# Kernel optimization log

Hardware: AMD Instinct MI355X
Metric: run time of the kernel (lower is better)

## Reference

```python
import jax, jax.numpy as jnp
import numpy as np

B, T, LAGS, H, F = 4096, 256, 32, 128, 2


def setup_inputs() -> dict:
    key = jax.random.key(0)
    ks = jax.random.split(key, 6)
    s = lambda n: 1.0 / np.sqrt(n)
    return {
        "inputs": jax.random.normal(ks[0], (B, T, F), jnp.float32),
        "Wx": jax.random.normal(ks[1], (F, H), jnp.float32) * s(F),
        "Wh": jax.random.normal(ks[2], (H, H), jnp.float32) * s(H),
        "b": jnp.zeros((H,), jnp.float32),
        "Wd": jax.random.normal(ks[3], (H, 1), jnp.float32) * s(H),
        "bd": jnp.zeros((1,), jnp.float32),
        "alpha": jax.random.uniform(ks[4], (1, 1), jnp.float32),
        "lags": LAGS,
    }


def reference(inputs, Wx, Wh, b, Wd, bd, alpha, lags):
    # alpha constrained to [0, 1] (MinMax constraint / clamp in call)
    a = jnp.clip(alpha, 0.0, 1.0)  # [1,1]
    Bsz = inputs.shape[0]
    h0 = jnp.zeros((Bsz, Wh.shape[0]), inputs.dtype)

    def cell(h, x):
        # SimpleRNN cell: tanh(x Wx + h Wh + b)
        return jnp.tanh(x @ Wx + h @ Wh + b)

    # ---- warmup: run RNN over first `lags` steps of the full 2-feature input
    warm_xs = jnp.transpose(inputs[:, :lags], (1, 0, 2))  # [lags, B, F]

    def warm_step(h, x):
        return cell(h, x), None

    h, _ = jax.lax.scan(warm_step, h0, warm_xs)
    pred = h @ Wd + bd  # [B, 1] first prediction (appended un-smoothed)

    # step n consumes exogenous inputs[:, lags + n - 1, 0]
    exog = jnp.transpose(inputs[:, lags:-1, 0])  # [T-lags-1, B]

    def ar_step(carry, e):
        h, pred, es = carry
        x = jnp.concatenate([e[:, None], pred], axis=-1)  # [B, 2]
        h = cell(h, x)
        pred = h @ Wd + bd
        es = a * pred + (1.0 - a) * es  # exponential smoothing blend
        return (h, pred, es), es

    _, es_seq = jax.lax.scan(ar_step, (h, pred, pred), exog)  # [T-lags-1, B, 1]

    preds = jnp.concatenate([pred[None], es_seq], axis=0)  # [T-lags, B, 1]
    return jnp.transpose(preds, (1, 0, 2))  # [B, T-lags, 1]
```

## Files before the change

### kernel.cpp

```cpp
#include <hip/hip_runtime.h>

namespace {

constexpr int kB = 4096;
constexpr int kT = 256;
constexpr int kLags = 32;
constexpr int kH = 128;
constexpr int kSteps = 255;
constexpr int kOut = 224;
constexpr int kMT = 16;
constexpr int kThreads = 512;
constexpr int kHS = 136;
constexpr int kOS = 225;

constexpr float kZS = 2.8853900817779268f;

typedef __attribute__((ext_vector_type(8))) short short8;
typedef __attribute__((ext_vector_type(4))) float f32x4;

struct __align__(16) SMem {
    unsigned short hhi[2][kMT][kHS];
    unsigned short hlo[2][kMT][kHS];
    float x0T[kT][kMT];
    float x1wT[kLags][kMT];
    float obuf[kMT][kOS];
};

__device__ __forceinline__ unsigned short bf16_rne(float f) {
    unsigned u = __builtin_bit_cast(unsigned, f);
    u += 0x7FFFu + ((u >> 16) & 1u);
    return (unsigned short)(u >> 16);
}
__device__ __forceinline__ float bf16_f32(unsigned short h) {
    unsigned u = ((unsigned)h) << 16;
    return __builtin_bit_cast(float, u);
}
__device__ __forceinline__ float tanh_from_zs(float zs) {
    float e = __builtin_amdgcn_exp2f(zs);
    return fmaf(-2.0f, __builtin_amdgcn_rcpf(e + 1.0f), 1.0f);
}
__device__ __forceinline__ unsigned bf16_rne_hibits(float f) {
    unsigned u = __builtin_bit_cast(unsigned, f);
    return (u + (0x7FFFu + ((u >> 16) & 1u))) & 0xFFFF0000u;
}

__global__ __launch_bounds__(kThreads, 2)
void arx_rnn_es_kernel(const float* __restrict__ inputs,
                       const float* __restrict__ Wx,
                       const float* __restrict__ Wh,
                       const float* __restrict__ bias,
                       const float* __restrict__ Wd,
                       const float* __restrict__ bd,
                       const float* __restrict__ alpha,
                       float* __restrict__ out) {
    __shared__ SMem sm;
    const int tid  = threadIdx.x;
    const int b0   = blockIdx.x * kMT;
    const int lane = tid & 63;
    const int w    = tid >> 6;
    const int n    = lane & 15;
    const int q    = lane >> 4;

    for (int idx = tid; idx < kMT * kT; idx += kThreads) {
        const int mm = idx >> 8;
        const int t  = idx & 255;
        float2 v = ((const float2*)inputs)[(size_t)(b0 + mm) * kT + t];
        sm.x0T[t][mm] = v.x;
        if (t < kLags) sm.x1wT[t][mm] = v.y;
    }
    for (int idx = tid; idx < kMT * kHS; idx += kThreads) {
        ((unsigned short*)sm.hhi[0])[idx] = 0;
        ((unsigned short*)sm.hlo[0])[idx] = 0;
    }

    const float av  = fminf(fmaxf(alpha[0], 0.0f), 1.0f);
    const float bdv = bd[0];

    float sb2[4], swx0[4], swx1e[4], sbp[4];
#pragma unroll
    for (int r = 0; r < 4; ++r) {
        const int colE = w * 16 + q * 4 + r;
        const float bc = bias[colE];
        const float w0 = Wx[colE];
        const float w1 = Wx[kH + colE];
        sb2[r]   = kZS * bc;
        swx0[r]  = kZS * w0;
        swx1e[r] = kZS * w1;
        sbp[r]   = kZS * (bc + bdv * w1);
    }
    __syncthreads();

    int p = 0;

    {
        short8 whh[4], whl[4];
        {
            const int colw = w * 16 + n;
#pragma unroll
            for (int c = 0; c < 4; ++c) {
#pragma unroll
                for (int j = 0; j < 8; ++j) {
                    const int k = c * 32 + q * 8 + j;
                    float wv = kZS * Wh[(size_t)k * kH + colw];
                    unsigned short hi = bf16_rne(wv);
                    whh[c][j] = (short)hi;
                    whl[c][j] = (short)bf16_rne(wv - bf16_f32(hi));
                }
            }
        }

#pragma unroll 1
        for (int st = 0; st < kLags; ++st) {
            const float x0s = sm.x0T[st][n];
            const float x1s = sm.x1wT[st][n];

            short8 bh[4], bl[4];
#pragma unroll
            for (int c = 0; c < 4; ++c) {
                bh[c] = *(const short8*)&sm.hhi[p][n][c * 32 + 8 * q];
                bl[c] = *(const short8*)&sm.hlo[p][n][c * 32 + 8 * q];
            }

            f32x4 A = *(const f32x4*)&sb2[0];
#pragma unroll
            for (int c = 0; c < 4; ++c) {
                A = __builtin_amdgcn_mfma_f32_16x16x32_bf16(whh[c], bh[c], A, 0, 0, 0);
                A = __builtin_amdgcn_mfma_f32_16x16x32_bf16(whl[c], bh[c], A, 0, 0, 0);
                A = __builtin_amdgcn_mfma_f32_16x16x32_bf16(whh[c], bl[c], A, 0, 0, 0);
            }

            unsigned rb[4], db[4];
#pragma unroll
            for (int r = 0; r < 4; ++r) {
                float zs = A[r] + x0s * swx0[r] + x1s * swx1e[r];
                float hf = tanh_from_zs(zs);
                rb[r] = bf16_rne_hibits(hf);
                float d = hf - __builtin_bit_cast(float, rb[r]);
                db[r] = __builtin_bit_cast(unsigned, d);
            }
            uint2 uh, ul;
            uh.x = __builtin_amdgcn_perm(rb[1], rb[0], 0x07060302u);
            uh.y = __builtin_amdgcn_perm(rb[3], rb[2], 0x07060302u);
            ul.x = __builtin_amdgcn_perm(db[1], db[0], 0x07060302u);
            ul.y = __builtin_amdgcn_perm(db[3], db[2], 0x07060302u);
            const int wcol = w * 16 + q * 4;
            *(uint2*)&sm.hhi[1 - p][n][wcol] = uh;
            *(uint2*)&sm.hlo[1 - p][n][wcol] = ul;

            __syncthreads();
            p ^= 1;
        }
    }

    short8 fhh[4], fhl[4], dh[4];
    {
        const int colw = w * 16 + n;
        const float wx1w = Wx[kH + colw];
#pragma unroll
        for (int c = 0; c < 4; ++c) {
#pragma unroll
            for (int j = 0; j < 8; ++j) {
                const int k = c * 32 + q * 8 + j;
                float wv = kZS * fmaf(Wd[k], wx1w, Wh[(size_t)k * kH + colw]);
                unsigned short hi = bf16_rne(wv);
                fhh[c][j] = (short)hi;
                fhl[c][j] = (short)bf16_rne(wv - bf16_f32(hi));
                dh[c][j]  = (short)bf16_rne(Wd[k]);
            }
        }
    }

    float es = 0.0f;

#pragma unroll 1
    for (int st = kLags; st < kSteps; ++st) {
        const float x0s = sm.x0T[st][n];

        short8 bh[4], bl[4];
#pragma unroll
        for (int c = 0; c < 4; ++c) {
            bh[c] = *(const short8*)&sm.hhi[p][n][c * 32 + 8 * q];
            bl[c] = *(const short8*)&sm.hlo[p][n][c * 32 + 8 * q];
        }

        f32x4 A = *(const f32x4*)&sbp[0];
        f32x4 P = {0, 0, 0, 0};
#pragma unroll
        for (int c = 0; c < 4; ++c) {
            A = __builtin_amdgcn_mfma_f32_16x16x32_bf16(fhh[c], bh[c], A, 0, 0, 0);
            A = __builtin_amdgcn_mfma_f32_16x16x32_bf16(fhl[c], bh[c], A, 0, 0, 0);
            A = __builtin_amdgcn_mfma_f32_16x16x32_bf16(fhh[c], bl[c], A, 0, 0, 0);
            if (w == 0)
                P = __builtin_amdgcn_mfma_f32_16x16x32_bf16(dh[c], bh[c], P, 0, 0, 0);
        }

        if (w == 0 && q == 0) {
            float pv = P[0] + bdv;
            es = (st == kLags) ? pv : fmaf(av, pv - es, es);
            sm.obuf[n][st - kLags] = es;
        }

        unsigned rb[4], db[4];
#pragma unroll
        for (int r = 0; r < 4; ++r) {
            float zs = A[r] + x0s * swx0[r];
            float hf = tanh_from_zs(zs);
            rb[r] = bf16_rne_hibits(hf);
            float d = hf - __builtin_bit_cast(float, rb[r]);
            db[r] = __builtin_bit_cast(unsigned, d);
        }
        uint2 uh, ul;
        uh.x = __builtin_amdgcn_perm(rb[1], rb[0], 0x07060302u);
        uh.y = __builtin_amdgcn_perm(rb[3], rb[2], 0x07060302u);
        ul.x = __builtin_amdgcn_perm(db[1], db[0], 0x07060302u);
        ul.y = __builtin_amdgcn_perm(db[3], db[2], 0x07060302u);
        const int wcol = w * 16 + q * 4;
        *(uint2*)&sm.hhi[1 - p][n][wcol] = uh;
        *(uint2*)&sm.hlo[1 - p][n][wcol] = ul;

        __syncthreads();
        p ^= 1;
    }

    if (w == 0) {
        f32x4 P = {0, 0, 0, 0};
#pragma unroll
        for (int c = 0; c < 4; ++c) {
            short8 bh = *(const short8*)&sm.hhi[p][n][c * 32 + 8 * q];
            P = __builtin_amdgcn_mfma_f32_16x16x32_bf16(dh[c], bh, P, 0, 0, 0);
        }
        if (q == 0) {
            float pv = P[0] + bdv;
            es = fmaf(av, pv - es, es);
            sm.obuf[n][kOut - 1] = es;
        }
    }

    __syncthreads();
    for (int idx = tid; idx < kMT * kOut; idx += kThreads) {
        const int mm = idx / kOut;
        const int t  = idx - mm * kOut;
        out[(size_t)(b0 + mm) * kOut + t] = sm.obuf[mm][t];
    }
}

}

extern "C" void kernel_launch(void* const* d_in, const int* in_sizes, int n_in,
                              void* d_out, int out_size, void* d_ws, size_t ws_size,
                              hipStream_t stream) {
    const float* inputs = (const float*)d_in[0];
    const float* Wx     = (const float*)d_in[1];
    const float* Wh     = (const float*)d_in[2];
    const float* bias   = (const float*)d_in[3];
    const float* Wd     = (const float*)d_in[4];
    const float* bd     = (const float*)d_in[5];
    const float* alpha  = (const float*)d_in[6];

    arx_rnn_es_kernel<<<kB / kMT, kThreads, 0, stream>>>(
        inputs, Wx, Wh, bias, Wd, bd, alpha, (float*)d_out);
}
```

Measured before the change: 206.0 us.

## Halve block to 4 waves, each computing two 16-column hidden tiles

The block shrinks from 8 to 4 wavefronts. Each wave now owns 32 hidden columns as two MFMA tiles, and both tiles reuse the same loaded h fragments from LDS. This halves the per-step LDS reads of h and the number of waves meeting at each per-step barrier, and gives two independent MFMA accumulation chains per wave to hide latency. In exchange, register pressure roughly doubles for the weight fragments, the launch_bounds occupancy hint is dropped, and fewer waves are available to hide latency on the serial recurrence.

```diff
diff --git a/kernel.cpp b/kernel.cpp
--- a/kernel.cpp
+++ b/kernel.cpp
@@ -9,7 +9,7 @@
 constexpr int kSteps = 255;
 constexpr int kOut = 224;
 constexpr int kMT = 16;
-constexpr int kThreads = 512;
+constexpr int kThreads = 256;
 constexpr int kHS = 136;
 constexpr int kOS = 225;
 
@@ -44,7 +44,7 @@
     return (u + (0x7FFFu + ((u >> 16) & 1u))) & 0xFFFF0000u;
 }
 
-__global__ __launch_bounds__(kThreads, 2)
+__global__ __launch_bounds__(kThreads)
 void arx_rnn_es_kernel(const float* __restrict__ inputs,
                        const float* __restrict__ Wx,
                        const float* __restrict__ Wh,
@@ -76,26 +76,30 @@
     const float av  = fminf(fmaxf(alpha[0], 0.0f), 1.0f);
     const float bdv = bd[0];
 
-    float sb2[4], swx0[4], swx1e[4], sbp[4];
-#pragma unroll
-    for (int r = 0; r < 4; ++r) {
-        const int colE = w * 16 + q * 4 + r;
-        const float bc = bias[colE];
-        const float w0 = Wx[colE];
-        const float w1 = Wx[kH + colE];
-        sb2[r]   = kZS * bc;
-        swx0[r]  = kZS * w0;
-        swx1e[r] = kZS * w1;
-        sbp[r]   = kZS * (bc + bdv * w1);
+    float sb2[2][4], swx0[2][4], swx1e[2][4], sbp[2][4];
+#pragma unroll
+    for (int t = 0; t < 2; ++t) {
+#pragma unroll
+        for (int r = 0; r < 4; ++r) {
+            const int colE = w * 32 + t * 16 + q * 4 + r;
+            const float bc = bias[colE];
+            const float w0 = Wx[colE];
+            const float w1 = Wx[kH + colE];
+            sb2[t][r]   = kZS * bc;
+            swx0[t][r]  = kZS * w0;
+            swx1e[t][r] = kZS * w1;
+            sbp[t][r]   = kZS * (bc + bdv * w1);
+        }
     }
     __syncthreads();
 
     int p = 0;
 
     {
-        short8 whh[4], whl[4];
-        {
-            const int colw = w * 16 + n;
+        short8 whh[2][4], whl[2][4];
+#pragma unroll
+        for (int t = 0; t < 2; ++t) {
+            const int colw = w * 32 + t * 16 + n;
 #pragma unroll
             for (int c = 0; c < 4; ++c) {
 #pragma unroll
@@ -103,8 +107,8 @@
                     const int k = c * 32 + q * 8 + j;
                     float wv = kZS * Wh[(size_t)k * kH + colw];
                     unsigned short hi = bf16_rne(wv);
-                    whh[c][j] = (short)hi;
-                    whl[c][j] = (short)bf16_rne(wv - bf16_f32(hi));
+                    whh[t][c][j] = (short)hi;
+                    whl[t][c][j] = (short)bf16_rne(wv - bf16_f32(hi));
                 }
             }
         }
@@ -121,18 +125,104 @@
                 bl[c] = *(const short8*)&sm.hlo[p][n][c * 32 + 8 * q];
             }
 
-            f32x4 A = *(const f32x4*)&sb2[0];
+            f32x4 A[2];
+#pragma unroll
+            for (int t = 0; t < 2; ++t) A[t] = *(const f32x4*)&sb2[t][0];
 #pragma unroll
             for (int c = 0; c < 4; ++c) {
-                A = __builtin_amdgcn_mfma_f32_16x16x32_bf16(whh[c], bh[c], A, 0, 0, 0);
-                A = __builtin_amdgcn_mfma_f32_16x16x32_bf16(whl[c], bh[c], A, 0, 0, 0);
-                A = __builtin_amdgcn_mfma_f32_16x16x32_bf16(whh[c], bl[c], A, 0, 0, 0);
-            }
-
+#pragma unroll
+                for (int t = 0; t < 2; ++t) {
+                    A[t] = __builtin_amdgcn_mfma_f32_16x16x32_bf16(whh[t][c], bh[c], A[t], 0, 0, 0);
+                    A[t] = __builtin_amdgcn_mfma_f32_16x16x32_bf16(whl[t][c], bh[c], A[t], 0, 0, 0);
+                    A[t] = __builtin_amdgcn_mfma_f32_16x16x32_bf16(whh[t][c], bl[c], A[t], 0, 0, 0);
+                }
+            }
+
+#pragma unroll
+            for (int t = 0; t < 2; ++t) {
+                unsigned rb[4], db[4];
+#pragma unroll
+                for (int r = 0; r < 4; ++r) {
+                    float zs = A[t][r] + x0s * swx0[t][r] + x1s * swx1e[t][r];
+                    float hf = tanh_from_zs(zs);
+                    rb[r] = bf16_rne_hibits(hf);
+                    float d = hf - __builtin_bit_cast(float, rb[r]);
+                    db[r] = __builtin_bit_cast(unsigned, d);
+                }
+                uint2 uh, ul;
+                uh.x = __builtin_amdgcn_perm(rb[1], rb[0], 0x07060302u);
+                uh.y = __builtin_amdgcn_perm(rb[3], rb[2], 0x07060302u);
+                ul.x = __builtin_amdgcn_perm(db[1], db[0], 0x07060302u);
+                ul.y = __builtin_amdgcn_perm(db[3], db[2], 0x07060302u);
+                const int wcol = w * 32 + t * 16 + q * 4;
+                *(uint2*)&sm.hhi[1 - p][n][wcol] = uh;
+                *(uint2*)&sm.hlo[1 - p][n][wcol] = ul;
+            }
+            __syncthreads();
+            p ^= 1;
+        }
+    }
+
+    short8 fhh[2][4], fhl[2][4], dh[4];
+#pragma unroll
+    for (int t = 0; t < 2; ++t) {
+        const int colw = w * 32 + t * 16 + n;
+        const float wx1w = Wx[kH + colw];
+#pragma unroll
+        for (int c = 0; c < 4; ++c) {
+#pragma unroll
+            for (int j = 0; j < 8; ++j) {
+                const int k = c * 32 + q * 8 + j;
+                float wv = kZS * fmaf(Wd[k], wx1w, Wh[(size_t)k * kH + colw]);
+                unsigned short hi = bf16_rne(wv);
+                fhh[t][c][j] = (short)hi;
+                fhl[t][c][j] = (short)bf16_rne(wv - bf16_f32(hi));
+                if (t == 0) dh[c][j] = (short)bf16_rne(Wd[k]);
+            }
+        }
+    }
+
+    float es = 0.0f;
+
+#pragma unroll 1
+    for (int st = kLags; st < kSteps; ++st) {
+        const float x0s = sm.x0T[st][n];
+
+        short8 bh[4], bl[4];
+#pragma unroll
+        for (int c = 0; c < 4; ++c) {
+            bh[c] = *(const short8*)&sm.hhi[p][n][c * 32 + 8 * q];
+            bl[c] = *(const short8*)&sm.hlo[p][n][c * 32 + 8 * q];
+        }
+
+        f32x4 A[2];
+#pragma unroll
+        for (int t = 0; t < 2; ++t) A[t] = *(const f32x4*)&sbp[t][0];
+        f32x4 P = {0, 0, 0, 0};
+#pragma unroll
+        for (int c = 0; c < 4; ++c) {
+#pragma unroll
+            for (int t = 0; t < 2; ++t) {
+                A[t] = __builtin_amdgcn_mfma_f32_16x16x32_bf16(fhh[t][c], bh[c], A[t], 0, 0, 0);
+                A[t] = __builtin_amdgcn_mfma_f32_16x16x32_bf16(fhl[t][c], bh[c], A[t], 0, 0, 0);
+                A[t] = __builtin_amdgcn_mfma_f32_16x16x32_bf16(fhh[t][c], bl[c], A[t], 0, 0, 0);
+            }
+            if (w == 0)
+                P = __builtin_amdgcn_mfma_f32_16x16x32_bf16(dh[c], bh[c], P, 0, 0, 0);
+        }
+
+        if (w == 0 && q == 0) {
+            float pv = P[0] + bdv;
+            es = (st == kLags) ? pv : fmaf(av, pv - es, es);
+            sm.obuf[n][st - kLags] = es;
+        }
+
+#pragma unroll
+        for (int t = 0; t < 2; ++t) {
             unsigned rb[4], db[4];
 #pragma unroll
             for (int r = 0; r < 4; ++r) {
-                float zs = A[r] + x0s * swx0[r] + x1s * swx1e[r];
+                float zs = A[t][r] + x0s * swx0[t][r];
                 float hf = tanh_from_zs(zs);
                 rb[r] = bf16_rne_hibits(hf);
                 float d = hf - __builtin_bit_cast(float, rb[r]);
@@ -143,80 +233,10 @@
             uh.y = __builtin_amdgcn_perm(rb[3], rb[2], 0x07060302u);
             ul.x = __builtin_amdgcn_perm(db[1], db[0], 0x07060302u);
             ul.y = __builtin_amdgcn_perm(db[3], db[2], 0x07060302u);
-            const int wcol = w * 16 + q * 4;
+            const int wcol = w * 32 + t * 16 + q * 4;
             *(uint2*)&sm.hhi[1 - p][n][wcol] = uh;
             *(uint2*)&sm.hlo[1 - p][n][wcol] = ul;
-
-            __syncthreads();
-            p ^= 1;
-        }
-    }
-
-    short8 fhh[4], fhl[4], dh[4];
-    {
-        const int colw = w * 16 + n;
-        const float wx1w = Wx[kH + colw];
-#pragma unroll
-        for (int c = 0; c < 4; ++c) {
-#pragma unroll
-            for (int j = 0; j < 8; ++j) {
-                const int k = c * 32 + q * 8 + j;
-                float wv = kZS * fmaf(Wd[k], wx1w, Wh[(size_t)k * kH + colw]);
-                unsigned short hi = bf16_rne(wv);
-                fhh[c][j] = (short)hi;
-                fhl[c][j] = (short)bf16_rne(wv - bf16_f32(hi));
-                dh[c][j]  = (short)bf16_rne(Wd[k]);
-            }
-        }
-    }
-
-    float es = 0.0f;
-
-#pragma unroll 1
-    for (int st = kLags; st < kSteps; ++st) {
-        const float x0s = sm.x0T[st][n];
-
-        short8 bh[4], bl[4];
-#pragma unroll
-        for (int c = 0; c < 4; ++c) {
-            bh[c] = *(const short8*)&sm.hhi[p][n][c * 32 + 8 * q];
-            bl[c] = *(const short8*)&sm.hlo[p][n][c * 32 + 8 * q];
-        }
-
-        f32x4 A = *(const f32x4*)&sbp[0];
-        f32x4 P = {0, 0, 0, 0};
-#pragma unroll
-        for (int c = 0; c < 4; ++c) {
-            A = __builtin_amdgcn_mfma_f32_16x16x32_bf16(fhh[c], bh[c], A, 0, 0, 0);
-            A = __builtin_amdgcn_mfma_f32_16x16x32_bf16(fhl[c], bh[c], A, 0, 0, 0);
-            A = __builtin_amdgcn_mfma_f32_16x16x32_bf16(fhh[c], bl[c], A, 0, 0, 0);
-            if (w == 0)
-                P = __builtin_amdgcn_mfma_f32_16x16x32_bf16(dh[c], bh[c], P, 0, 0, 0);
-        }
-
-        if (w == 0 && q == 0) {
-            float pv = P[0] + bdv;
-            es = (st == kLags) ? pv : fmaf(av, pv - es, es);
-            sm.obuf[n][st - kLags] = es;
-        }
-
-        unsigned rb[4], db[4];
-#pragma unroll
-        for (int r = 0; r < 4; ++r) {
-            float zs = A[r] + x0s * swx0[r];
-            float hf = tanh_from_zs(zs);
-            rb[r] = bf16_rne_hibits(hf);
-            float d = hf - __builtin_bit_cast(float, rb[r]);
-            db[r] = __builtin_bit_cast(unsigned, d);
-        }
-        uint2 uh, ul;
-        uh.x = __builtin_amdgcn_perm(rb[1], rb[0], 0x07060302u);
-        uh.y = __builtin_amdgcn_perm(rb[3], rb[2], 0x07060302u);
-        ul.x = __builtin_amdgcn_perm(db[1], db[0], 0x07060302u);
-        ul.y = __builtin_amdgcn_perm(db[3], db[2], 0x07060302u);
-        const int wcol = w * 16 + q * 4;
-        *(uint2*)&sm.hhi[1 - p][n][wcol] = uh;
-        *(uint2*)&sm.hlo[1 - p][n][wcol] = ul;
+        }
 
         __syncthreads();
         p ^= 1;
```

Result: slower. 231.3 us (+12.3%).
